# Kernel optimization log

Hardware: AMD Instinct MI355X
Metric: run time of the kernel (lower is better)

Reference implementation:

```python
import jax, jax.numpy as jnp
import numpy as np

N, E, G = 50000, 800000, 64
IN, HID, H, OUT = 128, 64, 4, 10


def _gat_layer(x, src, dst, W, a_src, a_dst, b):
    # x: [N, Fin]; W: [H*C, Fin]; a_src/a_dst: [H, C]; b: [H*C]
    n = x.shape[0]
    C = a_src.shape[1]
    h = (x @ W.T).reshape(n, H, C)                      # [N, H, C]
    e_src = jnp.einsum('nhc,hc->nh', h, a_src)          # [N, H]
    e_dst = jnp.einsum('nhc,hc->nh', h, a_dst)          # [N, H]
    logits = jax.nn.leaky_relu(e_src[src] + e_dst[dst], 0.2)  # [E', H]
    # segment softmax over destination node
    m = jax.ops.segment_max(logits, dst, num_segments=n)
    ex = jnp.exp(logits - m[dst])
    denom = jax.ops.segment_sum(ex, dst, num_segments=n)
    alpha = ex / (denom[dst] + 1e-16)                   # [E', H]
    msg = h[src] * alpha[:, :, None]                    # [E', H, C]
    out = jax.ops.segment_sum(msg, dst, num_segments=n) # [N, H, C]
    return out.reshape(n, H * C) + b


def setup_inputs() -> dict:
    key = jax.random.key(0)
    ks = jax.random.split(key, 20)
    x = jax.random.normal(ks[0], (N, IN), dtype=jnp.float32)
    edge_index = jax.random.randint(ks[1], (2, E), 0, N, dtype=jnp.int64)
    batch = jnp.sort(jax.random.randint(ks[2], (N,), 0, G, dtype=jnp.int64))

    def glorot(k, shape):
        fan = shape[-1]
        return jax.random.normal(k, shape, dtype=jnp.float32) / jnp.sqrt(jnp.float32(fan))

    ins = [IN, HID * H, HID * H]
    params = {}
    for i, fin in enumerate(ins, start=1):
        params[f'W{i}'] = glorot(ks[3 * i], (H * HID, fin))
        params[f'a_src{i}'] = glorot(ks[3 * i + 1], (H, HID))
        params[f'a_dst{i}'] = glorot(ks[3 * i + 2], (H, HID))
        params[f'b{i}'] = jnp.zeros((H * HID,), dtype=jnp.float32)
    params['Wl'] = glorot(ks[13], (OUT, H * HID))
    params['bl'] = jnp.zeros((OUT,), dtype=jnp.float32)
    return dict(x=x, edge_index=edge_index, batch=batch, **params)


def reference(x, edge_index, batch,
              W1, a_src1, a_dst1, b1,
              W2, a_src2, a_dst2, b2,
              W3, a_src3, a_dst3, b3,
              Wl, bl):
    n = x.shape[0]
    loops = jnp.arange(n, dtype=edge_index.dtype)
    src = jnp.concatenate([edge_index[0], loops])  # add self-loops (PyG default)
    dst = jnp.concatenate([edge_index[1], loops])

    h = jax.nn.elu(_gat_layer(x, src, dst, W1, a_src1, a_dst1, b1))
    h = jax.nn.elu(_gat_layer(h, src, dst, W2, a_src2, a_dst2, b2))
    h = _gat_layer(h, src, dst, W3, a_src3, a_dst3, b3)

    # global mean pool over graphs
    sums = jax.ops.segment_sum(h, batch, num_segments=G)          # [G, H*HID]
    counts = jax.ops.segment_sum(jnp.ones((n,), h.dtype), batch, num_segments=G)
    pooled = sums / jnp.maximum(counts, 1.0)[:, None]
    return pooled @ Wl.T + bl                                      # [G, OUT]
```

## Files before the change

kernel.cpp:

```cpp
#include <hip/hip_runtime.h>
#include <hip/hip_bf16.h>
#include <math.h>

#define NNODES 50000
#define NEDGES 800000
#define NGRAPH 64
#define FIN 128
#define HC 256
#define NHEAD 4
#define NOUT 10
#define ETOT (NEDGES + NNODES)
#define NB196 ((NNODES + 255) / 256)
#define BCAP 5376
#define S1CHUNK 4096
#define NBS1 ((ETOT + S1CHUNK - 1) / S1CHUNK)


typedef unsigned short u16;
typedef unsigned char u8;
typedef __attribute__((ext_vector_type(8))) short short8;
typedef __attribute__((ext_vector_type(4))) float f32x4;
typedef __attribute__((ext_vector_type(2))) float f32x2;
typedef __attribute__((ext_vector_type(4))) unsigned uint4v;

__device__ inline u16 f2b(float f) {
    union { float f; unsigned u; } v; v.f = f;
    unsigned r = v.u + 0x7FFF + ((v.u >> 16) & 1);
    return (u16)(r >> 16);
}
__device__ inline float b2f(u16 u) {
    union { unsigned u; float f; } v; v.u = ((unsigned)u) << 16; return v.f;
}

__device__ inline void gload_lds16(const void* g, void* l) {
    __builtin_amdgcn_global_load_lds(
        (const __attribute__((address_space(1))) unsigned*)g,
        (__attribute__((address_space(3))) unsigned*)l, 16, 0, 0);
}


#define CS0 (NNODES * FIN)
#define CS1 (HC * FIN)
#define CS2 (HC * HC)
#define NBCONV (((CS0 + CS1 + 2 * CS2) / 4 + 255) / 256)

__global__ void prep_kernel(const float* __restrict__ x, const float* __restrict__ W1,
                            const float* __restrict__ W2, const float* __restrict__ W3,
                            u16* __restrict__ xb, u16* __restrict__ w1b,
                            u16* __restrict__ w2b, u16* __restrict__ w3b) {
    int b = blockIdx.x;
    long i = (long)(b * 256 + threadIdx.x) * 4;
    if (i < CS0) {
        float4 v = *(const float4*)(x + i);
        ushort4 o;
        o.x = f2b(v.x); o.y = f2b(v.y); o.z = f2b(v.z); o.w = f2b(v.w);
        *(ushort4*)(xb + i) = o;
    } else if (i < CS0 + CS1) {
        long off = i - CS0;
        float4 v = *(const float4*)(W1 + off);
        ushort4 o;
        o.x = f2b(v.x); o.y = f2b(v.y); o.z = f2b(v.z); o.w = f2b(v.w);
        *(ushort4*)(w1b + off) = o;
    } else if (i < CS0 + CS1 + 2 * CS2) {
        const float* src; u16* dst; long off;
        if (i < CS0 + CS1 + CS2) { src = W2; dst = w2b; off = i - CS0 - CS1; }
        else                     { src = W3; dst = w3b; off = i - CS0 - CS1 - CS2; }
        float4 v = *(const float4*)(src + off);
        int row = (int)(off >> 8), col = (int)(off & 255);
        float vv[4] = {v.x, v.y, v.z, v.w};
        #pragma unroll
        for (int k = 0; k < 4; ++k) {
            int c = col + k;
            int pp = (c & ~63) | ((c & 15) << 2) | ((c >> 4) & 3);
            dst[row * 256 + pp] = f2b(vv[k]);
        }
    }
}


__global__ __launch_bounds__(256) void scatter1_kernel(const int* __restrict__ ei,
                                                       int* __restrict__ bcur,
                                                       unsigned* __restrict__ tmp) {
    __shared__ int hist[NB196];
    __shared__ int basec[NB196];
    int tid = threadIdx.x;
    int e0 = blockIdx.x * S1CHUNK;
    for (int i = tid; i < NB196; i += 256) hist[i] = 0;
    __syncthreads();
    int bkt[16], rnk[16];
    unsigned pk[16];
    #pragma unroll
    for (int k = 0; k < 16; ++k) {
        int e = e0 + k * 256 + tid;
        bkt[k] = -1;
        if (e < ETOT) {
            int src, dstn;
            if (e < NEDGES) { src = ei[e]; dstn = ei[NEDGES + e]; }
            else            { src = dstn = e - NEDGES; }
            int b = dstn >> 8;
            bkt[k] = b;
            rnk[k] = atomicAdd(&hist[b], 1);
            pk[k] = (unsigned)src | ((unsigned)(dstn & 255) << 16);
        }
    }
    __syncthreads();
    for (int i = tid; i < NB196; i += 256) {
        int h = hist[i];
        basec[i] = h ? atomicAdd(&bcur[i], h) : 0;
    }
    __syncthreads();
    #pragma unroll
    for (int k = 0; k < 16; ++k) {
        if (bkt[k] >= 0) {
            int pos = basec[bkt[k]] + rnk[k];
            if (pos < BCAP)
                tmp[(size_t)bkt[k] * BCAP + pos] = pk[k];
        }
    }
}


__global__ __launch_bounds__(256) void scanb_kernel(const int* __restrict__ bcur,
                                                    int* __restrict__ bsum,
                                                    const int* __restrict__ batch,
                                                    int* __restrict__ goff) {
    int tid = threadIdx.x, lane = tid & 63, wid = tid >> 6;
    __shared__ int ws[4];
    int v = 0;
    if (tid < NB196) { v = bcur[tid]; if (v > BCAP) v = BCAP; }
    int x = v;
    #pragma unroll
    for (int o = 1; o < 64; o <<= 1) {
        int t = __shfl_up(x, o);
        if (lane >= o) x += t;
    }
    if (lane == 63) ws[wid] = x;
    __syncthreads();
    if (tid < 4) {
        int w = ws[tid];
        #pragma unroll
        for (int o = 1; o < 4; o <<= 1) {
            int t = __shfl_up(w, o, 4);
            if ((tid & 3) >= o) w += t;
        }
        ws[tid] = w;
    }
    __syncthreads();
    int wexcl = wid ? ws[wid - 1] : 0;
    if (tid <= NB196) bsum[tid] = x - v + wexcl;
    if (tid <= NGRAPH) {
        int g = tid, lo = 0, hi = NNODES;
        while (lo < hi) {
            int mid = (lo + hi) >> 1;
            if (batch[mid] < g) lo = mid + 1; else hi = mid;
        }
        goff[g] = lo;
    }
}


__global__ __launch_bounds__(256) void scatter2_kernel(const unsigned* __restrict__ tmp,
                                                       const int* __restrict__ bcur,
                                                       const int* __restrict__ bsum,
                                                       int* __restrict__ off,
                                                       int* __restrict__ ssrc) {
    __shared__ unsigned ebuf[BCAP];
    __shared__ int ldss[BCAP];
    __shared__ int cnt[256];
    __shared__ int loff[256];
    __shared__ int ws[4];
    int b = blockIdx.x;
    int tid = threadIdx.x;
    int n = bcur[b];
    if (n > BCAP) n = BCAP;
    cnt[tid] = 0;
    const unsigned* tb = tmp + (size_t)b * BCAP;
    for (int i = tid; i < n; i += 256) ebuf[i] = tb[i];
    __syncthreads();
    for (int i = tid; i < n; i += 256) atomicAdd(&cnt[ebuf[i] >> 16], 1);
    __syncthreads();
    int lane = tid & 63, wid = tid >> 6;
    int v = cnt[tid];
    int x = v;
    #pragma unroll
    for (int o = 1; o < 64; o <<= 1) {
        int t = __shfl_up(x, o);
        if (lane >= o) x += t;
    }
    if (lane == 63) ws[wid] = x;
    __syncthreads();
    if (tid < 4) {
        int w = ws[tid];
        #pragma unroll
        for (int o = 1; o < 4; o <<= 1) {
            int t = __shfl_up(w, o, 4);
            if ((tid & 3) >= o) w += t;
        }
        ws[tid] = w;
    }
    __syncthreads();
    int wexcl = wid ? ws[wid - 1] : 0;
    int excl = x - v + wexcl;
    loff[tid] = excl;
    off[b * 256 + tid] = excl;
    cnt[tid] = 0;
    __syncthreads();
    for (int i = tid; i < n; i += 256) {
        unsigned pk = ebuf[i];
        int ld = (int)(pk >> 16);
        int rank = atomicAdd(&cnt[ld], 1);
        ldss[loff[ld] + rank] = (int)(pk & 0xFFFFu);
    }
    __syncthreads();
    int s = bsum[b];
    for (int i = tid; i < n; i += 256) ssrc[s + i] = ldss[i];
}


#define TBM 128
#define TBN 128
#define TBK 32

__global__ __launch_bounds__(256) void gemm_mfma(const u16* __restrict__ A,
                                                 const u16* __restrict__ B,
                                                 u8* __restrict__ C, int K,
                                                 const float* __restrict__ asrc,
                                                 const float* __restrict__ adst,
                                                 float* __restrict__ es,
                                                 float* __restrict__ ed) {
    __shared__ u16 Als[TBM * TBK];
    __shared__ u16 Bls[TBN * TBK];
    int tid = threadIdx.x;
    int wave = tid >> 6, lane = tid & 63;
    int brow = blockIdx.x * TBM, bcol = blockIdx.y * TBN;
    int m_base = (wave >> 1) * 64, n_base = (wave & 1) * 64;
    int r0 = tid >> 2, kc = (tid & 3) * 8;
    int lquad = lane >> 4, l16 = lane & 15;

    f32x4 acc[4][4] = {};

    const u16* ga0 = A + (size_t)(brow + r0) * K + kc;
    const u16* ga1 = A + (size_t)(brow + 64 + r0) * K + kc;
    const u16* gb0 = B + (size_t)(bcol + r0) * K + kc;
    const u16* gb1 = B + (size_t)(bcol + 64 + r0) * K + kc;
    u16* la0 = &Als[r0 * TBK + kc];
    u16* la1 = &Als[(64 + r0) * TBK + kc];
    u16* lb0 = &Bls[r0 * TBK + kc];
    u16* lb1 = &Bls[(64 + r0) * TBK + kc];

    for (int k0 = 0; k0 < K; k0 += TBK) {
        __syncthreads();
        gload_lds16(ga0 + k0, la0);
        gload_lds16(ga1 + k0, la1);
        gload_lds16(gb0 + k0, lb0);
        gload_lds16(gb1 + k0, lb1);
        __syncthreads();
        short8 fa[4], fb[4];
        #pragma unroll
        for (int i = 0; i < 4; ++i) {
            fa[i] = *(const short8*)(&Als[(m_base + i * 16 + l16) * TBK + lquad * 8]);
            fb[i] = *(const short8*)(&Bls[(n_base + i * 16 + l16) * TBK + lquad * 8]);
        }
        #pragma unroll
        for (int i = 0; i < 4; ++i)
            #pragma unroll
            for (int j = 0; j < 4; ++j)
                acc[i][j] = __builtin_amdgcn_mfma_f32_16x16x32_bf16(fa[i], fb[j], acc[i][j], 0, 0, 0);
    }

    #pragma unroll
    for (int i = 0; i < 4; ++i) {
        int rbase = brow + m_base + i * 16 + lquad * 4;
        #pragma unroll
        for (int r = 0; r < 4; ++r) {
            int row = rbase + r;
            if (row < NNODES) {
                int u = 0;
                u = __builtin_amdgcn_cvt_pk_fp8_f32(acc[i][0][r], acc[i][1][r], u, false);
                u = __builtin_amdgcn_cvt_pk_fp8_f32(acc[i][2][r], acc[i][3][r], u, true);
                *(int*)(C + (size_t)row * HC + bcol + n_base + l16 * 4) = u;
            }
        }
    }

    int head = (bcol + n_base) >> 6;
    float asv[4], adv[4];
    #pragma unroll
    for (int j = 0; j < 4; ++j) {
        asv[j] = asrc[head * 64 + j * 16 + l16];
        adv[j] = adst[head * 64 + j * 16 + l16];
    }
    #pragma unroll
    for (int i = 0; i < 4; ++i) {
        #pragma unroll
        for (int r = 0; r < 4; ++r) {
            float ps = 0.f, pd = 0.f;
            #pragma unroll
            for (int j = 0; j < 4; ++j) {
                ps = fmaf(acc[i][j][r], asv[j], ps);
                pd = fmaf(acc[i][j][r], adv[j], pd);
            }
            #pragma unroll
            for (int o = 1; o < 16; o <<= 1) {
                ps += __shfl_xor(ps, o);
                pd += __shfl_xor(pd, o);
            }
            int row = brow + m_base + i * 16 + lquad * 4 + r;
            if (l16 == 0 && row < NNODES) {
                es[row * 4 + head] = ps;
                ed[row * 4 + head] = pd;
            }
        }
    }
}


__global__ __launch_bounds__(256) void aggregate_kernel(const u8* __restrict__ h,
                                                        const int* __restrict__ ssrc,
                                                        const int* __restrict__ off,
                                                        const int* __restrict__ bsum,
                                                        const float* __restrict__ es,
                                                        const float* __restrict__ ed,
                                                        const float* __restrict__ bias,
                                                        u16* __restrict__ out,
                                                        int apply_elu) {
    __shared__ int2 xch[4][4][17];
    const uint4v* h128 = (const uint4v*)h;
    int wid = threadIdx.x >> 6;
    int dst = blockIdx.x * 4 + wid;
    if (dst >= NNODES) return;
    int lane = threadIdx.x & 63;
    int headp = lane >> 4;
    int j16 = lane & 15;
    int g = lane >> 4;
    int q = lane & 15;
    int headc = q >> 2;
    int s = off[dst] + bsum[dst >> 8];
    int e = off[dst + 1] + bsum[(dst + 1) >> 8];
    float edh = ed[dst * 4 + headp];
    int2* pslot = &xch[wid][headp][0];
    const int2* cslot = &xch[wid][headc][0];

    float acc[16] = {};
    float dpriv = 0.f;

    for (int base = s; base < e; base += 16) {
        int cnt = e - base;
        if (cnt > 16) cnt = 16;
        int mysrc = 0;
        float myex = 0.f;
        if (j16 < cnt) {
            mysrc = ssrc[base + j16];
            float l = es[mysrc * 4 + headp] + edh;
            l = fmaxf(l, 0.2f * l);
            myex = __expf(l);
            dpriv += myex;
        }
        pslot[j16] = make_int2(mysrc, __float_as_int(myex));
        #pragma unroll
        for (int j = 0; j < 4; ++j) {
            if (j * 4 >= cnt) break;
            int2 pr = cslot[j * 4 + g];
            float exj = __int_as_float(pr.y);
            uint4v hv = h128[(((unsigned)pr.x) << 4) + (unsigned)q];
            #pragma unroll
            for (int u = 0; u < 4; ++u) {
                f32x2 lo = __builtin_amdgcn_cvt_pk_f32_fp8(hv[u], false);
                f32x2 hi = __builtin_amdgcn_cvt_pk_f32_fp8(hv[u], true);
                acc[u * 4 + 0] += lo.x * exj;
                acc[u * 4 + 1] += lo.y * exj;
                acc[u * 4 + 2] += hi.x * exj;
                acc[u * 4 + 3] += hi.y * exj;
            }
        }
    }

    #pragma unroll
    for (int o = 1; o < 16; o <<= 1) dpriv += __shfl_xor(dpriv, o);
    float inv = 1.f / (dpriv + 1e-16f);
    float invc = __shfl(inv, headc << 4);

    #pragma unroll
    for (int k = 0; k < 8; ++k) {
        float snd = (lane & 32) ? acc[k] : acc[k + 8];
        float rcv = __shfl_xor(snd, 32);
        if (lane & 32) acc[k + 8] += rcv; else acc[k] += rcv;
    }
    #pragma unroll
    for (int k = 0; k < 8; ++k)
        if (lane & 32) acc[k] = acc[k + 8];
    #pragma unroll
    for (int k = 0; k < 4; ++k) {
        float snd = (lane & 16) ? acc[k] : acc[k + 4];
        float rcv = __shfl_xor(snd, 16);
        if (lane & 16) acc[k + 4] += rcv; else acc[k] += rcv;
    }
    #pragma unroll
    for (int k = 0; k < 4; ++k)
        if (lane & 16) acc[k] = acc[k + 4];

    int cbase = headc * 64 + (q & 3) * 4 + g;
    float o0 = acc[0] * invc + bias[cbase];
    float o1 = acc[1] * invc + bias[cbase + 16];
    float o2 = acc[2] * invc + bias[cbase + 32];
    float o3 = acc[3] * invc + bias[cbase + 48];
    if (apply_elu) {
        o0 = o0 > 0.f ? o0 : __expf(o0) - 1.f;
        o1 = o1 > 0.f ? o1 : __expf(o1) - 1.f;
        o2 = o2 > 0.f ? o2 : __expf(o2) - 1.f;
        o3 = o3 > 0.f ? o3 : __expf(o3) - 1.f;
    }
    ushort4 ov;
    ov.x = f2b(o0); ov.y = f2b(o1); ov.z = f2b(o2); ov.w = f2b(o3);
    *(ushort4*)(out + (size_t)dst * HC + q * 16 + g * 4) = ov;
}


__global__ __launch_bounds__(256) void pool_kernel(const u16* __restrict__ hin,
                                                   const int* __restrict__ goff,
                                                   float* __restrict__ pp) {
    int g = blockIdx.x;
    int slice = blockIdx.y;
    int lane = threadIdx.x & 63;
    int wid = threadIdx.x >> 6;
    int s = goff[g], e = goff[g + 1];
    float a0 = 0.f, a1 = 0.f, a2 = 0.f, a3 = 0.f;
    for (int n = s + slice * 4 + wid; n < e; n += 32) {
        ushort4 hv = *(const ushort4*)(hin + (size_t)n * HC + lane * 4);
        a0 += b2f(hv.x); a1 += b2f(hv.y); a2 += b2f(hv.z); a3 += b2f(hv.w);
    }
    __shared__ float4 part[4][64];
    part[wid][lane] = make_float4(a0, a1, a2, a3);
    __syncthreads();
    if (wid == 0) {
        float4 p0 = part[0][lane], p1 = part[1][lane], p2 = part[2][lane], p3 = part[3][lane];
        float4 v = make_float4((p0.x + p1.x) + (p2.x + p3.x),
                               (p0.y + p1.y) + (p2.y + p3.y),
                               (p0.z + p1.z) + (p2.z + p3.z),
                               (p0.w + p1.w) + (p2.w + p3.w));
        *(float4*)(pp + ((size_t)(g * 8 + slice)) * HC + lane * 4) = v;
    }
}


__global__ __launch_bounds__(64) void final_kernel(const float* __restrict__ pp,
                                                   const int* __restrict__ goff,
                                                   const float* __restrict__ Wl,
                                                   const float* __restrict__ bl,
                                                   float* __restrict__ out) {
    int g = blockIdx.x;
    int lane = threadIdx.x;
    float4 pv = make_float4(0.f, 0.f, 0.f, 0.f);
    #pragma unroll
    for (int sl = 0; sl < 8; ++sl) {
        float4 v = *(const float4*)(pp + ((size_t)(g * 8 + sl)) * HC + lane * 4);
        pv.x += v.x; pv.y += v.y; pv.z += v.z; pv.w += v.w;
    }
    float cntf = fmaxf((float)(goff[g + 1] - goff[g]), 1.f);
    float inv = 1.f / cntf;
    pv.x *= inv; pv.y *= inv; pv.z *= inv; pv.w *= inv;
    int wbase = ((lane >> 4) << 6) | (lane & 15);
    float acc[NOUT];
    #pragma unroll
    for (int o = 0; o < NOUT; ++o) {
        const float* w = Wl + o * HC + wbase;
        acc[o] = pv.x * w[0] + pv.y * w[16] + pv.z * w[32] + pv.w * w[48];
    }
    #pragma unroll
    for (int s = 32; s > 0; s >>= 1)
        #pragma unroll
        for (int o = 0; o < NOUT; ++o)
            acc[o] += __shfl_xor(acc[o], s);
    if (lane == 0) {
        #pragma unroll
        for (int o = 0; o < NOUT; ++o)
            out[g * NOUT + o] = acc[o] + bl[o];
    }
}


extern "C" void kernel_launch(void* const* d_in, const int* in_sizes, int n_in,
                              void* d_out, int out_size, void* d_ws, size_t ws_size,
                              hipStream_t stream) {
    (void)in_sizes; (void)n_in; (void)out_size; (void)ws_size;
    const float* x   = (const float*)d_in[0];
    const int*   ei  = (const int*)d_in[1];
    const int*   bat = (const int*)d_in[2];
    const float* W1  = (const float*)d_in[3];
    const float* as1 = (const float*)d_in[4];
    const float* ad1 = (const float*)d_in[5];
    const float* b1  = (const float*)d_in[6];
    const float* W2  = (const float*)d_in[7];
    const float* as2 = (const float*)d_in[8];
    const float* ad2 = (const float*)d_in[9];
    const float* b2  = (const float*)d_in[10];
    const float* W3  = (const float*)d_in[11];
    const float* as3 = (const float*)d_in[12];
    const float* ad3 = (const float*)d_in[13];
    const float* b3  = (const float*)d_in[14];
    const float* Wl  = (const float*)d_in[15];
    const float* bl  = (const float*)d_in[16];
    float* out = (float*)d_out;

    char* ws = (char*)d_ws;
    size_t p = 0;
    auto alloc = [&](size_t bytes) {
        size_t a = p;
        p += (bytes + 255) & ~(size_t)255;
        return a;
    };
    int*      off  = (int*)(ws + alloc((size_t)(NB196 * 256 + 256) * 4));
    int*      bcur = (int*)(ws + alloc(256 * 4));
    int*      ssrc = (int*)(ws + alloc((size_t)ETOT * 4));
    unsigned* tmp  = (unsigned*)(ws + alloc((size_t)NB196 * BCAP * 4));
    int*      bsum = (int*)(ws + alloc(256 * 4));
    float*    es   = (float*)(ws + alloc((size_t)NNODES * NHEAD * 4));
    float*    ed   = (float*)(ws + alloc((size_t)NNODES * NHEAD * 4));
    u16*      xb   = (u16*)(ws + alloc((size_t)NNODES * FIN * 2));
    u16*      w1b  = (u16*)(ws + alloc((size_t)HC * FIN * 2));
    u16*      w2b  = (u16*)(ws + alloc((size_t)HC * HC * 2));
    u16*      w3b  = (u16*)(ws + alloc((size_t)HC * HC * 2));
    u8*       Hb   = (u8*)(ws + alloc((size_t)NNODES * HC));
    u16*      Ab   = (u16*)(ws + alloc((size_t)NNODES * HC * 2));
    float*    pp   = (float*)(ws + alloc((size_t)NGRAPH * 8 * HC * 4));
    int*      goff = (int*)(ws + alloc((size_t)(NGRAPH + 1) * 4));
    alloc(128 * 1024);

    hipMemsetAsync(bcur, 0, 256 * 4, stream);

    prep_kernel<<<NBCONV, 256, 0, stream>>>(x, W1, W2, W3, xb, w1b, w2b, w3b);

    scatter1_kernel<<<NBS1, 256, 0, stream>>>(ei, bcur, tmp);
    scanb_kernel<<<1, 256, 0, stream>>>(bcur, bsum, bat, goff);
    scatter2_kernel<<<NB196, 256, 0, stream>>>(tmp, bcur, bsum, off, ssrc);

    dim3 ggrid((NNODES + TBM - 1) / TBM, HC / TBN);
    int nblocks4 = (NNODES + 3) / 4;

    gemm_mfma<<<ggrid, 256, 0, stream>>>(xb, w1b, Hb, FIN, as1, ad1, es, ed);
    aggregate_kernel<<<nblocks4, 256, 0, stream>>>(Hb, ssrc, off, bsum, es, ed, b1, Ab, 1);
    gemm_mfma<<<ggrid, 256, 0, stream>>>(Ab, w2b, Hb, HC, as2, ad2, es, ed);
    aggregate_kernel<<<nblocks4, 256, 0, stream>>>(Hb, ssrc, off, bsum, es, ed, b2, Ab, 1);
    gemm_mfma<<<ggrid, 256, 0, stream>>>(Ab, w3b, Hb, HC, as3, ad3, es, ed);
    aggregate_kernel<<<nblocks4, 256, 0, stream>>>(Hb, ssrc, off, bsum, es, ed, b3, Ab, 0);

    dim3 pgrid(NGRAPH, 8);
    pool_kernel<<<pgrid, 256, 0, stream>>>(Ab, goff, pp);
    final_kernel<<<NGRAPH, 64, 0, stream>>>(pp, goff, Wl, bl, out);
}
```

Before: 356.9 us.

## Rework GAT aggregation to one-edge-per-wave gathers with software-pipelined logits

The aggregation kernel drops the 4-edges-per-wave 16-byte gathers and the cross-lane shuffle reduction that followed them. Each wave now walks edges one at a time, with every lane loading 4 bytes of the source row, so each lane keeps 4 accumulators that already line up with the output channels. Edge indices and attention exponentials are double-buffered in LDS and prefetched one or two chunks ahead, so index and logit loads overlap the gather loop. The trade is more serial iterations with smaller, less vectorised loads in exchange for fewer registers, no reduction epilogue and hidden index latency.

```diff
diff --git a/kernel.cpp b/kernel.cpp
--- a/kernel.cpp
+++ b/kernel.cpp
@@ -21,7 +21,6 @@
 typedef __attribute__((ext_vector_type(8))) short short8;
 typedef __attribute__((ext_vector_type(4))) float f32x4;
 typedef __attribute__((ext_vector_type(2))) float f32x2;
-typedef __attribute__((ext_vector_type(4))) unsigned uint4v;
 
 __device__ inline u16 f2b(float f) {
     union { float f; unsigned u; } v; v.f = f;
@@ -324,86 +323,73 @@
                                                         const float* __restrict__ bias,
                                                         u16* __restrict__ out,
                                                         int apply_elu) {
-    __shared__ int2 xch[4][4][17];
-    const uint4v* h128 = (const uint4v*)h;
+    __shared__ int2 xch[4][4][2][17];
+    const unsigned* h32 = (const unsigned*)h;
     int wid = threadIdx.x >> 6;
     int dst = blockIdx.x * 4 + wid;
     if (dst >= NNODES) return;
     int lane = threadIdx.x & 63;
-    int headp = lane >> 4;
+    int head = lane >> 4;
     int j16 = lane & 15;
-    int g = lane >> 4;
-    int q = lane & 15;
-    int headc = q >> 2;
     int s = off[dst] + bsum[dst >> 8];
     int e = off[dst + 1] + bsum[(dst + 1) >> 8];
-    float edh = ed[dst * 4 + headp];
-    int2* pslot = &xch[wid][headp][0];
-    const int2* cslot = &xch[wid][headc][0];
-
-    float acc[16] = {};
-    float dpriv = 0.f;
-
+    float edh = ed[dst * 4 + head];
+
+    float a0 = 0.f, a1 = 0.f, a2 = 0.f, a3 = 0.f, dpriv = 0.f;
+
+    {
+        int cnt0 = e - s; if (cnt0 > 16) cnt0 = 16;
+        int idx0 = s + j16; if (idx0 >= ETOT) idx0 = 0;
+        int src0 = ssrc[idx0];
+        float l = es[src0 * 4 + head] + edh;
+        l = fmaxf(l, 0.2f * l);
+        float ex0 = 0.f;
+        if (j16 < cnt0) { ex0 = __expf(l); dpriv += ex0; }
+        xch[wid][head][0][j16] = make_int2(src0, __float_as_int(ex0));
+    }
+    int nidx = s + 16 + j16; if (nidx >= ETOT) nidx = 0;
+    int nsrc = ssrc[nidx];
+
+    int buf = 0;
     for (int base = s; base < e; base += 16) {
-        int cnt = e - base;
-        if (cnt > 16) cnt = 16;
-        int mysrc = 0;
-        float myex = 0.f;
-        if (j16 < cnt) {
-            mysrc = ssrc[base + j16];
-            float l = es[mysrc * 4 + headp] + edh;
+        int cur = e - base; if (cur > 16) cur = 16;
+        int nbase = base + 16;
+        float esv = es[(unsigned)nsrc * 4 + head];
+        int n2idx = base + 32 + j16; if (n2idx >= ETOT) n2idx = 0;
+        int n2src = ssrc[n2idx];
+        const int2* slot = &xch[wid][head][buf][0];
+        for (int j = 0; j < cur; ++j) {
+            int2 pr = slot[j];
+            float exj = __int_as_float(pr.y);
+            unsigned hv = h32[(unsigned)pr.x * 64 + lane];
+            f32x2 lo = __builtin_amdgcn_cvt_pk_f32_fp8(hv, false);
+            f32x2 hi = __builtin_amdgcn_cvt_pk_f32_fp8(hv, true);
+            a0 += lo.x * exj;
+            a1 += lo.y * exj;
+            a2 += hi.x * exj;
+            a3 += hi.y * exj;
+        }
+        if (nbase < e) {
+            int ncnt = e - nbase; if (ncnt > 16) ncnt = 16;
+            float l = esv + edh;
             l = fmaxf(l, 0.2f * l);
-            myex = __expf(l);
-            dpriv += myex;
-        }
-        pslot[j16] = make_int2(mysrc, __float_as_int(myex));
-        #pragma unroll
-        for (int j = 0; j < 4; ++j) {
-            if (j * 4 >= cnt) break;
-            int2 pr = cslot[j * 4 + g];
-            float exj = __int_as_float(pr.y);
-            uint4v hv = h128[(((unsigned)pr.x) << 4) + (unsigned)q];
-            #pragma unroll
-            for (int u = 0; u < 4; ++u) {
-                f32x2 lo = __builtin_amdgcn_cvt_pk_f32_fp8(hv[u], false);
-                f32x2 hi = __builtin_amdgcn_cvt_pk_f32_fp8(hv[u], true);
-                acc[u * 4 + 0] += lo.x * exj;
-                acc[u * 4 + 1] += lo.y * exj;
-                acc[u * 4 + 2] += hi.x * exj;
-                acc[u * 4 + 3] += hi.y * exj;
-            }
-        }
+            float nex = 0.f;
+            if (j16 < ncnt) { nex = __expf(l); dpriv += nex; }
+            xch[wid][head][buf ^ 1][j16] = make_int2(nsrc, __float_as_int(nex));
+        }
+        nsrc = n2src;
+        buf ^= 1;
     }
 
     #pragma unroll
     for (int o = 1; o < 16; o <<= 1) dpriv += __shfl_xor(dpriv, o);
     float inv = 1.f / (dpriv + 1e-16f);
-    float invc = __shfl(inv, headc << 4);
-
-    #pragma unroll
-    for (int k = 0; k < 8; ++k) {
-        float snd = (lane & 32) ? acc[k] : acc[k + 8];
-        float rcv = __shfl_xor(snd, 32);
-        if (lane & 32) acc[k + 8] += rcv; else acc[k] += rcv;
-    }
-    #pragma unroll
-    for (int k = 0; k < 8; ++k)
-        if (lane & 32) acc[k] = acc[k + 8];
-    #pragma unroll
-    for (int k = 0; k < 4; ++k) {
-        float snd = (lane & 16) ? acc[k] : acc[k + 4];
-        float rcv = __shfl_xor(snd, 16);
-        if (lane & 16) acc[k + 4] += rcv; else acc[k] += rcv;
-    }
-    #pragma unroll
-    for (int k = 0; k < 4; ++k)
-        if (lane & 16) acc[k] = acc[k + 4];
-
-    int cbase = headc * 64 + (q & 3) * 4 + g;
-    float o0 = acc[0] * invc + bias[cbase];
-    float o1 = acc[1] * invc + bias[cbase + 16];
-    float o2 = acc[2] * invc + bias[cbase + 32];
-    float o3 = acc[3] * invc + bias[cbase + 48];
+    int bbase = ((lane >> 4) << 6) | (lane & 15);
+    float b0 = bias[bbase], b1 = bias[bbase + 16], b2 = bias[bbase + 32], b3 = bias[bbase + 48];
+    float o0 = a0 * inv + b0;
+    float o1 = a1 * inv + b1;
+    float o2 = a2 * inv + b2;
+    float o3 = a3 * inv + b3;
     if (apply_elu) {
         o0 = o0 > 0.f ? o0 : __expf(o0) - 1.f;
         o1 = o1 > 0.f ? o1 : __expf(o1) - 1.f;
@@ -412,7 +398,7 @@
     }
     ushort4 ov;
     ov.x = f2b(o0); ov.y = f2b(o1); ov.z = f2b(o2); ov.w = f2b(o3);
-    *(ushort4*)(out + (size_t)dst * HC + q * 16 + g * 4) = ov;
+    *(ushort4*)(out + (size_t)dst * HC + lane * 4) = ov;
 }
 
 
```

Result: faster. 338.7 us (-5.1%).
